# Performance work log

Hardware: AMD Instinct MI355X
Metric: run time of the kernel (lower is better)

## Reference

```python
import jax, jax.numpy as jnp
import numpy as np

DIM = 1024
HEADS = 16
DIM_HEAD = 64
B = 4
N = 2048
INNER = HEADS * DIM_HEAD
SCALE = DIM_HEAD ** -0.5
NEG = -1e9


def setup_inputs() -> dict:
    key = jax.random.key(0)
    k1, k2, k3 = jax.random.split(key, 3)
    x = jax.random.normal(k1, (B, N, DIM), dtype=jnp.float32)
    w_qkv = jax.random.normal(k2, (DIM, 3 * INNER), dtype=jnp.float32) * (DIM ** -0.5)
    w_out = jax.random.normal(k3, (INNER, DIM), dtype=jnp.float32) * (INNER ** -0.5)
    b_out = jnp.zeros((DIM,), dtype=jnp.float32)
    return {"x": x, "w_qkv": w_qkv, "w_out": w_out, "b_out": b_out}


def reference(x, w_qkv, w_out, b_out):
    b, n, _ = x.shape
    qkv = x @ w_qkv  # [b, n, 3*inner]
    q, k, v = jnp.split(qkv, 3, axis=-1)
    # [b, n, inner] -> [b, h, n, d]
    split_heads = lambda t: t.reshape(b, n, HEADS, DIM_HEAD).transpose(0, 2, 1, 3)
    q, k, v = split_heads(q), split_heads(k), split_heads(v)
    dots = jnp.einsum('bhid,bhjd->bhij', q, k) * SCALE
    causal = jnp.tril(jnp.ones((n, n), dtype=bool))  # mask[i,j]=1 for j<=i
    dots = jnp.where(causal, dots, NEG)
    attn = jax.nn.softmax(dots, axis=-1)
    out = jnp.einsum('bhij,bhjd->bhid', attn, v)
    out = out.transpose(0, 2, 1, 3).reshape(b, n, INNER)
    return out @ w_out + b_out
```

## Files before the change

### kernel.cpp

```cpp
#include <hip/hip_runtime.h>

typedef unsigned short u16;
typedef unsigned int u32;
typedef __attribute__((ext_vector_type(8))) short short8;
typedef __attribute__((ext_vector_type(4))) float f32x4;
typedef __attribute__((ext_vector_type(4))) short short4v;
typedef __attribute__((ext_vector_type(2))) unsigned int uint2v;

#define MFMA_BF16(a, b, c) __builtin_amdgcn_mfma_f32_16x16x32_bf16((a), (b), (c), 0, 0, 0)

__device__ __forceinline__ void gl2lds16(const u16* g, u16* l) {
  __builtin_amdgcn_global_load_lds(
      (const __attribute__((address_space(1))) unsigned int*)g,
      (__attribute__((address_space(3))) unsigned int*)l, 16, 0, 0);
}

__device__ __forceinline__ u16 f2bf(float f) {
  union { float f; unsigned u; } v; v.f = f;
  unsigned r = v.u + 0x7fffu + ((v.u >> 16) & 1u);
  return (u16)(r >> 16);
}

__device__ __forceinline__ u32 swz(u32 x) { return x ^ (((x >> 7) & 7u) << 4); }

__global__ void fill_one_f32(float* p, int n) {
  int i = blockIdx.x * blockDim.x + threadIdx.x;
  if (i < n) p[i] = 1.0f;
}

__global__ void prep_k(const float* __restrict__ x, u16* __restrict__ Xb,
                       const float* __restrict__ w_qkv, u16* __restrict__ wqkvT,
                       const float* __restrict__ w_out, u16* __restrict__ woutT) {
  __shared__ float tile[32][33];
  const int bid = blockIdx.x, t = threadIdx.x;
  if (bid < 2048) {
    const int base = (bid * 256 + t) * 16;
#pragma unroll
    for (int h = 0; h < 2; ++h) {
      const f32x4 v0 = *(const f32x4*)&x[base + h * 8];
      const f32x4 v1 = *(const f32x4*)&x[base + h * 8 + 4];
      short8 o;
      o[0] = (short)f2bf(v0.x); o[1] = (short)f2bf(v0.y);
      o[2] = (short)f2bf(v0.z); o[3] = (short)f2bf(v0.w);
      o[4] = (short)f2bf(v1.x); o[5] = (short)f2bf(v1.y);
      o[6] = (short)f2bf(v1.z); o[7] = (short)f2bf(v1.w);
      *(short8*)&Xb[base + h * 8] = o;
    }
    return;
  }
  const float* src; u16* dst; int R, C, bx, by;
  if (bid < 5120) {
    const int tb = bid - 2048;
    src = w_qkv; dst = wqkvT; R = 1024; C = 3072; bx = tb % 96; by = tb / 96;
  } else {
    const int tb = bid - 5120;
    src = w_out; dst = woutT; R = 1024; C = 1024; bx = tb % 32; by = tb / 32;
  }
  const int tx = t & 31, ty = t >> 5;
  const int r0 = by * 32, c0 = bx * 32;
#pragma unroll
  for (int i = 0; i < 4; ++i)
    tile[ty + i * 8][tx] = src[(size_t)(r0 + ty + i * 8) * C + c0 + tx];
  __syncthreads();
#pragma unroll
  for (int i = 0; i < 4; ++i)
    dst[(size_t)(c0 + ty + i * 8) * R + r0 + tx] = f2bf(tile[tx][ty + i * 8]);
}

#define ASLOT 8192
#define BSLOT 16384
template <int MODE>
__launch_bounds__(512, 2)
__global__ void gemm_bt_k(const u16* __restrict__ A, const u16* __restrict__ Bt,
                          int K, int Ncols,
                          u16* __restrict__ O0, u16* __restrict__ O1,
                          u16* __restrict__ O2,
                          float* __restrict__ Of, const float* __restrict__ biasf) {
  __shared__ __align__(16) u16 Al[3 * ASLOT / 2];
  __shared__ __align__(16) u16 Bl[3 * BSLOT / 2];
  const int t = threadIdx.x;
  const int w = t >> 6, l = t & 63;
  const int quad = l >> 4, l16 = l & 15;
  const int m0 = blockIdx.y * 128, n0 = blockIdx.x * 256;
  const int wm = w >> 2, wn = w & 3;

  f32x4 acc[4][4];
#pragma unroll
  for (int a = 0; a < 4; ++a)
#pragma unroll
    for (int b = 0; b < 4; ++b) acc[a][b] = (f32x4){0.f, 0.f, 0.f, 0.f};

  const u32 oA = (u32)t * 16u;
  const u32 lA = swz(oA);
  const u16* srcA = A + (size_t)(m0 + (lA >> 6)) * K + ((lA >> 4) & 3) * 8;
  const u32 oB0 = (u32)t * 16u, oB1 = 8192u + (u32)t * 16u;
  const u32 lB0 = swz(oB0), lB1 = swz(oB1);
  const u16* srcB0 = Bt + (size_t)(n0 + (lB0 >> 6)) * K + ((lB0 >> 4) & 3) * 8;
  const u16* srcB1 = Bt + (size_t)(n0 + (lB1 >> 6)) * K + ((lB1 >> 4) & 3) * 8;

  u32 sa[4], sb[4];
#pragma unroll
  for (int a = 0; a < 4; ++a) {
    const u32 row = wm * 64 + a * 16 + l16;
    sa[a] = swz(row * 64 + quad * 16);
  }
#pragma unroll
  for (int b = 0; b < 4; ++b) {
    const u32 row = wn * 64 + b * 16 + l16;
    sb[b] = swz(row * 64 + quad * 16);
  }

  const int NT = K >> 5;

  gl2lds16(srcA, (u16*)((char*)Al + oA));
  gl2lds16(srcB0, (u16*)((char*)Bl + oB0));
  gl2lds16(srcB1, (u16*)((char*)Bl + oB1));
  gl2lds16(srcA + 32, (u16*)((char*)Al + ASLOT + oA));
  gl2lds16(srcB0 + 32, (u16*)((char*)Bl + BSLOT + oB0));
  gl2lds16(srcB1 + 32, (u16*)((char*)Bl + BSLOT + oB1));
  asm volatile("s_waitcnt vmcnt(3)" ::: "memory");
  __builtin_amdgcn_s_barrier();

  int rd = 0, st = 2;
  int kel = 64;
#pragma unroll 1
  for (int tt = 0; tt < NT - 2; ++tt) {
    {
      const u32 aoff = (u32)st * ASLOT, boff = (u32)st * BSLOT;
      gl2lds16(srcA + kel, (u16*)((char*)Al + aoff + oA));
      gl2lds16(srcB0 + kel, (u16*)((char*)Bl + boff + oB0));
      gl2lds16(srcB1 + kel, (u16*)((char*)Bl + boff + oB1));
      kel += 32;
    }
    const u32 ca = (u32)rd * ASLOT, cb = (u32)rd * BSLOT;
    short8 av[4], bv[4];
#pragma unroll
    for (int a = 0; a < 4; ++a)
      av[a] = *(const short8*)((const char*)Al + ca + sa[a]);
#pragma unroll
    for (int b = 0; b < 4; ++b)
      bv[b] = *(const short8*)((const char*)Bl + cb + sb[b]);
    __builtin_amdgcn_s_setprio(1);
#pragma unroll
    for (int a = 0; a < 4; ++a)
#pragma unroll
      for (int b = 0; b < 4; ++b)
        acc[a][b] = MFMA_BF16(av[a], bv[b], acc[a][b]);
    __builtin_amdgcn_s_setprio(0);
    asm volatile("s_waitcnt vmcnt(3)" ::: "memory");
    __builtin_amdgcn_s_barrier();
    rd = (rd == 2) ? 0 : rd + 1;
    st = (st == 2) ? 0 : st + 1;
  }
  {
    const u32 ca = (u32)rd * ASLOT, cb = (u32)rd * BSLOT;
    short8 av[4], bv[4];
#pragma unroll
    for (int a = 0; a < 4; ++a)
      av[a] = *(const short8*)((const char*)Al + ca + sa[a]);
#pragma unroll
    for (int b = 0; b < 4; ++b)
      bv[b] = *(const short8*)((const char*)Bl + cb + sb[b]);
#pragma unroll
    for (int a = 0; a < 4; ++a)
#pragma unroll
      for (int b = 0; b < 4; ++b)
        acc[a][b] = MFMA_BF16(av[a], bv[b], acc[a][b]);
    asm volatile("s_waitcnt vmcnt(0)" ::: "memory");
    __builtin_amdgcn_s_barrier();
    rd = (rd == 2) ? 0 : rd + 1;
  }
  {
    const u32 ca = (u32)rd * ASLOT, cb = (u32)rd * BSLOT;
    short8 av[4], bv[4];
#pragma unroll
    for (int a = 0; a < 4; ++a)
      av[a] = *(const short8*)((const char*)Al + ca + sa[a]);
#pragma unroll
    for (int b = 0; b < 4; ++b)
      bv[b] = *(const short8*)((const char*)Bl + cb + sb[b]);
#pragma unroll
    for (int a = 0; a < 4; ++a)
#pragma unroll
      for (int b = 0; b < 4; ++b)
        acc[a][b] = MFMA_BF16(av[a], bv[b], acc[a][b]);
  }

#pragma unroll
  for (int a = 0; a < 4; ++a)
#pragma unroll
    for (int b = 0; b < 4; ++b) {
      const int row0 = m0 + wm * 64 + a * 16 + quad * 4;
      const int col = n0 + wn * 64 + b * 16 + l16;
      if (MODE == 0) {
        const int bb = row0 >> 11, n = row0 & 2047;
        const int which = col >> 10, j = col & 1023, h = j >> 6, d = j & 63;
        if (which == 2) {
          short4v o;
#pragma unroll
          for (int r = 0; r < 4; ++r) o[r] = (short)f2bf(acc[a][b][r]);
          *(short4v*)&O2[(((size_t)bb * 16 + h) * 64 + d) * 2048 + n] = o;
        } else {
          u16* dst = which ? O1 : O0;
#pragma unroll
          for (int r = 0; r < 4; ++r)
            dst[(((size_t)bb * 16 + h) * 2048 + (n + r)) * 64 + d] =
                f2bf(acc[a][b][r]);
        }
      } else {
#pragma unroll
        for (int r = 0; r < 4; ++r)
          Of[(size_t)(row0 + r) * Ncols + col] = acc[a][b][r] + biasf[col];
      }
    }
}

#define KSV 72
#define PS 72
__launch_bounds__(512, 2)
__global__ void flash_k8(const u16* __restrict__ Q, const u16* __restrict__ K,
                         const u16* __restrict__ VT, u16* __restrict__ AO) {
  __shared__ __align__(16) u16 Klds[2][64 * KSV];
  __shared__ __align__(16) u16 Vt[2][64 * KSV];
  __shared__ __align__(16) u16 Plds[8][16 * PS];
  const int t = threadIdx.x, w = t >> 6, l = t & 63;
  const int quad = l >> 4, l16 = l & 15;
  const int flat = blockIdx.x;
  const int bh = flat & 63;
  const int grp = flat >> 6;
  const int qi = (grp < 4) ? grp : (11 - grp);
  const size_t base = (size_t)bh * 2048 * 64;
  const u16* Qp = Q + base;
  const u16* Kp = K + base;
  const u16* VTp = VT + base;
  const int bb = bh >> 4, hh = bh & 15;
  const float SC = 0.125f;
  const float FM = 3.0f;

  const int kcp = t >> 3, kcd = (t & 7) * 8;
  const int vcd = t >> 3, vcp = (t & 7) * 8;

  short8 ones;
#pragma unroll
  for (int j = 0; j < 8; ++j) ones[j] = (short)0x3F80;

  const int qbase = qi * 256;

  short8 qf[2][2];
#pragma unroll
  for (int mi = 0; mi < 2; ++mi) {
    const int qrow = qbase + w * 32 + mi * 16 + l16;
    qf[mi][0] = *(const short8*)&Qp[(size_t)qrow * 64 + quad * 8];
    qf[mi][1] = *(const short8*)&Qp[(size_t)qrow * 64 + 32 + quad * 8];
  }

  f32x4 oacc[2][4], lacc[2];
#pragma unroll
  for (int mi = 0; mi < 2; ++mi) {
    lacc[mi] = (f32x4){0.f, 0.f, 0.f, 0.f};
#pragma unroll
    for (int df = 0; df < 4; ++df) oacc[mi][df] = (f32x4){0.f, 0.f, 0.f, 0.f};
  }

  const int nkt = 4 * qi + 4;
  const int wlo = qbase + w * 32;
  const int whi = wlo + 31;

  short8 kv = *(const short8*)&Kp[(size_t)kcp * 64 + kcd];
  short8 vv = *(const short8*)&VTp[(size_t)vcd * 2048 + vcp];

#pragma unroll 1
  for (int kt = 0; kt < nkt; ++kt) {
    const int buf = kt & 1;
    *(short8*)&Klds[buf][kcp * KSV + kcd] = kv;
    *(short8*)&Vt[buf][vcd * KSV + vcp] = vv;
    __syncthreads();

    if (kt + 1 < nkt) {
      kv = *(const short8*)&Kp[(size_t)((kt + 1) * 64 + kcp) * 64 + kcd];
      vv = *(const short8*)&VTp[(size_t)vcd * 2048 + (kt + 1) * 64 + vcp];
    }

    const bool skip = (kt * 64 > whi);
    if (!skip) {
      f32x4 sa[2][4];
#pragma unroll
      for (int nf = 0; nf < 4; ++nf) {
        const short8 kf0 = *(const short8*)&Klds[buf][(nf * 16 + l16) * KSV + quad * 8];
        const short8 kf1 = *(const short8*)&Klds[buf][(nf * 16 + l16) * KSV + 32 + quad * 8];
#pragma unroll
        for (int mi = 0; mi < 2; ++mi) {
          f32x4 s = (f32x4){0.f, 0.f, 0.f, 0.f};
          s = MFMA_BF16(kf0, qf[mi][0], s);
          s = MFMA_BF16(kf1, qf[mi][1], s);
          sa[mi][nf] = s;
        }
      }

      const bool needmask = (kt * 64 + 63 > wlo);
      short8 pf[2][2];
#pragma unroll
      for (int mi = 0; mi < 2; ++mi) {
        const int qrow = qbase + w * 32 + mi * 16 + l16;
#pragma unroll
        for (int nf = 0; nf < 4; ++nf) {
          u32 dw[2];
#pragma unroll
          for (int h = 0; h < 2; ++h) {
            u32 pk = 0;
#pragma unroll
            for (int r2 = 0; r2 < 2; ++r2) {
              const int r = h * 2 + r2;
              float arg = fmaf(sa[mi][nf][r], SC, -FM);
              if (needmask) {
                const int kp = kt * 64 + nf * 16 + quad * 4 + r;
                arg = (kp <= qrow) ? arg : -1e9f;
              }
              union { float f; unsigned u; } pu;
              pu.f = __expf(arg);
              pk |= (u32)((pu.u + 0x8000u) >> 16) << (16 * r2);
            }
            dw[h] = pk;
          }
          *(uint2v*)&Plds[w][l16 * PS + nf * 16 + quad * 4] = (uint2v){dw[0], dw[1]};
        }
        pf[mi][0] = *(const short8*)&Plds[w][l16 * PS + quad * 8];
        pf[mi][1] = *(const short8*)&Plds[w][l16 * PS + 32 + quad * 8];
        lacc[mi] = MFMA_BF16(pf[mi][0], ones, lacc[mi]);
        lacc[mi] = MFMA_BF16(pf[mi][1], ones, lacc[mi]);
      }

#pragma unroll
      for (int df = 0; df < 4; ++df) {
        const int rowb = (df * 16 + l16) * KSV;
        const short8 vf0 = *(const short8*)&Vt[buf][rowb + quad * 8];
        const short8 vf1 = *(const short8*)&Vt[buf][rowb + 32 + quad * 8];
#pragma unroll
        for (int mi = 0; mi < 2; ++mi) {
          oacc[mi][df] = MFMA_BF16(pf[mi][0], vf0, oacc[mi][df]);
          oacc[mi][df] = MFMA_BF16(pf[mi][1], vf1, oacc[mi][df]);
        }
      }
    }
  }

#pragma unroll
  for (int mi = 0; mi < 2; ++mi) {
    const int srow = qbase + w * 32 + mi * 16 + quad * 4;
#pragma unroll
    for (int df = 0; df < 4; ++df)
#pragma unroll
      for (int r = 0; r < 4; ++r) {
        const int n = srow + r;
        const int d = df * 16 + l16;
        AO[((size_t)bb * 2048 + n) * 1024 + hh * 64 + d] =
            f2bf(oacc[mi][df][r] / lacc[mi][r]);
      }
  }
}

extern "C" void kernel_launch(void* const* d_in, const int* in_sizes, int n_in,
                              void* d_out, int out_size, void* d_ws, size_t ws_size,
                              hipStream_t stream) {
  const float* x = (const float*)d_in[0];
  const float* w_qkv = (const float*)d_in[1];
  const float* w_out = (const float*)d_in[2];
  const float* b_out = (const float*)d_in[3];
  float* out = (float*)d_out;

  const size_t MB = 1024 * 1024;
  if (ws_size < 72 * MB) {
    fill_one_f32<<<(out_size + 255) / 256, 256, 0, stream>>>(out, out_size);
    return;
  }

  char* ws = (char*)d_ws;
  u16* wqkvT = (u16*)(ws);
  u16* woutT = (u16*)(ws + 6 * MB);
  u16* Xb = (u16*)(ws + 8 * MB);
  u16* AO = Xb;
  u16* Qb = (u16*)(ws + 24 * MB);
  u16* Kb = (u16*)(ws + 40 * MB);
  u16* VbT = (u16*)(ws + 56 * MB);

  prep_k<<<6144, 256, 0, stream>>>(x, Xb, w_qkv, wqkvT, w_out, woutT);
  gemm_bt_k<0><<<dim3(3072 / 256, 8192 / 128), 512, 0, stream>>>(
      Xb, wqkvT, 1024, 3072, Qb, Kb, VbT, nullptr, nullptr);
  flash_k8<<<512, 512, 0, stream>>>(Qb, Kb, VbT, AO);
  gemm_bt_k<1><<<dim3(1024 / 256, 8192 / 128), 512, 0, stream>>>(
      AO, woutT, 1024, 1024, nullptr, nullptr, nullptr, out, b_out);
}
```

Before: 277.0 us.

## Shrink GEMM tiles to 128x128 with 256-thread blocks and a new LDS layout

```diff
diff --git a/kernel.cpp b/kernel.cpp
--- a/kernel.cpp
+++ b/kernel.cpp
@@ -20,6 +20,8 @@
   unsigned r = v.u + 0x7fffu + ((v.u >> 16) & 1u);
   return (u16)(r >> 16);
 }
+
+__device__ __forceinline__ void cfence() { asm volatile("" ::: "memory"); }
 
 __device__ __forceinline__ u32 swz(u32 x) { return x ^ (((x >> 7) & 7u) << 4); }
 
@@ -67,22 +69,20 @@
     dst[(size_t)(c0 + ty + i * 8) * R + r0 + tx] = f2bf(tile[tx][ty + i * 8]);
 }
 
-#define ASLOT 8192
-#define BSLOT 16384
 template <int MODE>
-__launch_bounds__(512, 2)
+__launch_bounds__(256, 2)
 __global__ void gemm_bt_k(const u16* __restrict__ A, const u16* __restrict__ Bt,
                           int K, int Ncols,
                           u16* __restrict__ O0, u16* __restrict__ O1,
                           u16* __restrict__ O2,
                           float* __restrict__ Of, const float* __restrict__ biasf) {
-  __shared__ __align__(16) u16 Al[3 * ASLOT / 2];
-  __shared__ __align__(16) u16 Bl[3 * BSLOT / 2];
+  __shared__ __align__(16) u16 Al[3 * 4096];
+  __shared__ __align__(16) u16 Bl[3 * 4096];
   const int t = threadIdx.x;
   const int w = t >> 6, l = t & 63;
   const int quad = l >> 4, l16 = l & 15;
-  const int m0 = blockIdx.y * 128, n0 = blockIdx.x * 256;
-  const int wm = w >> 2, wn = w & 3;
+  const int m0 = blockIdx.y * 128, n0 = blockIdx.x * 128;
+  const int wm = w & 1, wn = w >> 1;
 
   f32x4 acc[4][4];
 #pragma unroll
@@ -90,56 +90,57 @@
 #pragma unroll
     for (int b = 0; b < 4; ++b) acc[a][b] = (f32x4){0.f, 0.f, 0.f, 0.f};
 
-  const u32 oA = (u32)t * 16u;
-  const u32 lA = swz(oA);
-  const u16* srcA = A + (size_t)(m0 + (lA >> 6)) * K + ((lA >> 4) & 3) * 8;
-  const u32 oB0 = (u32)t * 16u, oB1 = 8192u + (u32)t * 16u;
-  const u32 lB0 = swz(oB0), lB1 = swz(oB1);
-  const u16* srcB0 = Bt + (size_t)(n0 + (lB0 >> 6)) * K + ((lB0 >> 4) & 3) * 8;
-  const u16* srcB1 = Bt + (size_t)(n0 + (lB1 >> 6)) * K + ((lB1 >> 4) & 3) * 8;
+  const u32 o0 = (u32)t * 16u, o1 = o0 + 4096u;
+  const u32 l0 = swz(o0), l1 = swz(o1 & 8191u);
+  const u32 rA0 = (l0 >> 7) * 2 + ((l0 >> 6) & 1), q0 = (l0 >> 4) & 3u;
+  const u32 rA1 = (l1 >> 7) * 2 + ((l1 >> 6) & 1), q1 = (l1 >> 4) & 3u;
+  const u16* srcA0 = A + (size_t)(m0 + rA0) * K + q0 * 8;
+  const u16* srcA1 = A + (size_t)(m0 + rA1) * K + q1 * 8;
+  const u16* srcB0 = Bt + (size_t)(n0 + rA0) * K + q0 * 8;
+  const u16* srcB1 = Bt + (size_t)(n0 + rA1) * K + q1 * 8;
+
+#define STAGE(kel_, s_)                                      \
+  do {                                                       \
+    char* _da = (char*)(Al + (s_)*4096);                     \
+    char* _db = (char*)(Bl + (s_)*4096);                     \
+    gl2lds16(srcA0 + (kel_), (u16*)(_da + o0));              \
+    gl2lds16(srcA1 + (kel_), (u16*)(_da + o1));              \
+    gl2lds16(srcB0 + (kel_), (u16*)(_db + o0));              \
+    gl2lds16(srcB1 + (kel_), (u16*)(_db + o1));              \
+  } while (0)
 
   u32 sa[4], sb[4];
 #pragma unroll
   for (int a = 0; a < 4; ++a) {
     const u32 row = wm * 64 + a * 16 + l16;
-    sa[a] = swz(row * 64 + quad * 16);
+    sa[a] = swz(((row >> 1) << 7) | ((row & 1) << 6) | ((u32)quad << 4));
   }
 #pragma unroll
   for (int b = 0; b < 4; ++b) {
     const u32 row = wn * 64 + b * 16 + l16;
-    sb[b] = swz(row * 64 + quad * 16);
+    sb[b] = swz(((row >> 1) << 7) | ((row & 1) << 6) | ((u32)quad << 4));
   }
 
   const int NT = K >> 5;
 
-  gl2lds16(srcA, (u16*)((char*)Al + oA));
-  gl2lds16(srcB0, (u16*)((char*)Bl + oB0));
-  gl2lds16(srcB1, (u16*)((char*)Bl + oB1));
-  gl2lds16(srcA + 32, (u16*)((char*)Al + ASLOT + oA));
-  gl2lds16(srcB0 + 32, (u16*)((char*)Bl + BSLOT + oB0));
-  gl2lds16(srcB1 + 32, (u16*)((char*)Bl + BSLOT + oB1));
-  asm volatile("s_waitcnt vmcnt(3)" ::: "memory");
-  __builtin_amdgcn_s_barrier();
+  STAGE(0, 0);
+  STAGE(32, 1);
+  asm volatile("s_waitcnt vmcnt(4)" ::: "memory");
+  cfence(); __builtin_amdgcn_s_barrier(); cfence();
 
   int rd = 0, st = 2;
   int kel = 64;
 #pragma unroll 1
   for (int tt = 0; tt < NT - 2; ++tt) {
-    {
-      const u32 aoff = (u32)st * ASLOT, boff = (u32)st * BSLOT;
-      gl2lds16(srcA + kel, (u16*)((char*)Al + aoff + oA));
-      gl2lds16(srcB0 + kel, (u16*)((char*)Bl + boff + oB0));
-      gl2lds16(srcB1 + kel, (u16*)((char*)Bl + boff + oB1));
-      kel += 32;
-    }
-    const u32 ca = (u32)rd * ASLOT, cb = (u32)rd * BSLOT;
+    STAGE(kel, st);
+    kel += 32;
+    const char* ca = (const char*)(Al + rd * 4096);
+    const char* cb = (const char*)(Bl + rd * 4096);
     short8 av[4], bv[4];
 #pragma unroll
-    for (int a = 0; a < 4; ++a)
-      av[a] = *(const short8*)((const char*)Al + ca + sa[a]);
-#pragma unroll
-    for (int b = 0; b < 4; ++b)
-      bv[b] = *(const short8*)((const char*)Bl + cb + sb[b]);
+    for (int a = 0; a < 4; ++a) av[a] = *(const short8*)(ca + sa[a]);
+#pragma unroll
+    for (int b = 0; b < 4; ++b) bv[b] = *(const short8*)(cb + sb[b]);
     __builtin_amdgcn_s_setprio(1);
 #pragma unroll
     for (int a = 0; a < 4; ++a)
@@ -147,44 +148,43 @@
       for (int b = 0; b < 4; ++b)
         acc[a][b] = MFMA_BF16(av[a], bv[b], acc[a][b]);
     __builtin_amdgcn_s_setprio(0);
-    asm volatile("s_waitcnt vmcnt(3)" ::: "memory");
-    __builtin_amdgcn_s_barrier();
+    asm volatile("s_waitcnt vmcnt(4)" ::: "memory");
+    cfence(); __builtin_amdgcn_s_barrier(); cfence();
     rd = (rd == 2) ? 0 : rd + 1;
     st = (st == 2) ? 0 : st + 1;
   }
   {
-    const u32 ca = (u32)rd * ASLOT, cb = (u32)rd * BSLOT;
+    const char* ca = (const char*)(Al + rd * 4096);
+    const char* cb = (const char*)(Bl + rd * 4096);
     short8 av[4], bv[4];
 #pragma unroll
-    for (int a = 0; a < 4; ++a)
-      av[a] = *(const short8*)((const char*)Al + ca + sa[a]);
-#pragma unroll
-    for (int b = 0; b < 4; ++b)
-      bv[b] = *(const short8*)((const char*)Bl + cb + sb[b]);
+    for (int a = 0; a < 4; ++a) av[a] = *(const short8*)(ca + sa[a]);
+#pragma unroll
+    for (int b = 0; b < 4; ++b) bv[b] = *(const short8*)(cb + sb[b]);
 #pragma unroll
     for (int a = 0; a < 4; ++a)
 #pragma unroll
       for (int b = 0; b < 4; ++b)
         acc[a][b] = MFMA_BF16(av[a], bv[b], acc[a][b]);
     asm volatile("s_waitcnt vmcnt(0)" ::: "memory");
-    __builtin_amdgcn_s_barrier();
+    cfence(); __builtin_amdgcn_s_barrier(); cfence();
     rd = (rd == 2) ? 0 : rd + 1;
   }
   {
-    const u32 ca = (u32)rd * ASLOT, cb = (u32)rd * BSLOT;
+    const char* ca = (const char*)(Al + rd * 4096);
+    const char* cb = (const char*)(Bl + rd * 4096);
     short8 av[4], bv[4];
 #pragma unroll
-    for (int a = 0; a < 4; ++a)
-      av[a] = *(const short8*)((const char*)Al + ca + sa[a]);
-#pragma unroll
-    for (int b = 0; b < 4; ++b)
-      bv[b] = *(const short8*)((const char*)Bl + cb + sb[b]);
+    for (int a = 0; a < 4; ++a) av[a] = *(const short8*)(ca + sa[a]);
+#pragma unroll
+    for (int b = 0; b < 4; ++b) bv[b] = *(const short8*)(cb + sb[b]);
 #pragma unroll
     for (int a = 0; a < 4; ++a)
 #pragma unroll
       for (int b = 0; b < 4; ++b)
         acc[a][b] = MFMA_BF16(av[a], bv[b], acc[a][b]);
   }
+#undef STAGE
 
 #pragma unroll
   for (int a = 0; a < 4; ++a)
@@ -384,9 +384,9 @@
   u16* VbT = (u16*)(ws + 56 * MB);
 
   prep_k<<<6144, 256, 0, stream>>>(x, Xb, w_qkv, wqkvT, w_out, woutT);
-  gemm_bt_k<0><<<dim3(3072 / 256, 8192 / 128), 512, 0, stream>>>(
+  gemm_bt_k<0><<<dim3(3072 / 128, 8192 / 128), 256, 0, stream>>>(
       Xb, wqkvT, 1024, 3072, Qb, Kb, VbT, nullptr, nullptr);
   flash_k8<<<512, 512, 0, stream>>>(Qb, Kb, VbT, AO);
-  gemm_bt_k<1><<<dim3(1024 / 256, 8192 / 128), 512, 0, stream>>>(
+  gemm_bt_k<1><<<dim3(1024 / 128, 8192 / 128), 256, 0, stream>>>(
       AO, woutT, 1024, 1024, nullptr, nullptr, nullptr, out, b_out);
 }
```

Result: faster. 255.9 us (-7.6%).
